# Kernel optimization log

Hardware: AMD Instinct MI355X
Metric: run time of the kernel (lower is better)

## Reference

```python
import jax, jax.numpy as jnp
import numpy as np

N_NODES, N_EDGES, N_REL, F_DIM, N_HEAD, N_LAYERS = 20000, 100000, 1000, 128, 4, 4
NEG_SLOPE = 0.2  # PyG GATv2Conv default negative_slope


def _gatv2_layer(x, ea_full, src, dst, Wl, bl, Wr, br, We, att, bias):
    # x: [N, F]; ea_full: [Etot, F] edge attrs (incl. self-loop rows)
    N = x.shape[0]
    H, C = att.shape  # heads, out-dim per head
    xl = (x @ Wl + bl).reshape(N, H, C)          # source-side projection
    xr = (x @ Wr + br).reshape(N, H, C)          # target-side projection
    ee = (ea_full @ We).reshape(-1, H, C)        # [Etot, H, C] edge embedding
    # GATv2 scoring: leaky_relu(x_i + x_j + e) . att
    e = jax.nn.leaky_relu(xl[src] + xr[dst] + ee, NEG_SLOPE)
    logits = jnp.einsum('ehc,hc->eh', e, att)    # [Etot, H]
    # segment softmax over edges grouped by destination node
    m = jax.ops.segment_max(logits, dst, num_segments=N)
    p = jnp.exp(logits - m[dst])
    denom = jax.ops.segment_sum(p, dst, num_segments=N)
    alpha = p / denom[dst]                       # [Etot, H]
    out = jax.ops.segment_sum(alpha[:, :, None] * xl[src], dst, num_segments=N)
    return out.mean(axis=1) + bias               # concat=False -> head mean


def setup_inputs() -> dict:
    key = jax.random.key(0)
    ks = jax.random.split(key, 12)
    N, E, R, F, H, L = N_NODES, N_EDGES, N_REL, F_DIM, N_HEAD, N_LAYERS
    HC = H * F
    s = 1.0 / np.sqrt(F)
    return {
        'x': jax.random.normal(ks[0], (N, F), jnp.float32),
        'edge_index': jax.random.randint(ks[1], (2, E), 0, N, dtype=jnp.int32),
        'relations': jax.random.normal(ks[2], (R, F), jnp.float32),
        'relation_index': jax.random.randint(ks[3], (E,), 0, R, dtype=jnp.int32),
        'Wl': jax.random.normal(ks[4], (L, F, HC), jnp.float32) * s,
        'bl': jnp.zeros((L, HC), jnp.float32),
        'Wr': jax.random.normal(ks[5], (L, F, HC), jnp.float32) * s,
        'br': jnp.zeros((L, HC), jnp.float32),
        'We': jax.random.normal(ks[6], (L, F, HC), jnp.float32) * s,
        'att': jax.random.normal(ks[7], (L, H, F), jnp.float32) * s,
        'bias': jnp.zeros((L, F), jnp.float32),
    }


def reference(x, edge_index, relations, relation_index, Wl, bl, Wr, br, We, att, bias):
    N = x.shape[0]
    sl = jnp.arange(N, dtype=edge_index.dtype)
    src = jnp.concatenate([edge_index[0], sl])   # add_self_loops=True
    dst = jnp.concatenate([edge_index[1], sl])
    ea = relations[relation_index]               # [E, F]
    # self-loop edge_attr uses fill_value='mean' (PyG default)
    ea_mean = ea.mean(axis=0)
    ea_full = jnp.concatenate([ea, jnp.broadcast_to(ea_mean, (N, ea.shape[1]))])
    h = x
    for l in range(N_LAYERS):
        h = _gatv2_layer(h, ea_full, src, dst, Wl[l], bl[l], Wr[l], br[l], We[l], att[l], bias[l])
    return (h, relations)
```

## Files before the change

### kernel.cpp

```cpp
#include <hip/hip_runtime.h>
#include <hip/hip_bf16.h>

#define N_NODES   20000
#define N_EDGES   100000
#define N_REL     1000
#define F_DIM     128
#define N_HEAD    4
#define HC        512
#define HC2       256
#define N_LAYERS  4
#define REL_EXT_ROWS 1008
#define NEG_SLOPE 0.2f
#define PROJ_NODE_X 157

typedef __attribute__((ext_vector_type(8))) short short8;
typedef __attribute__((ext_vector_type(4))) float floatx4;

__device__ __forceinline__ float loadIn(const void* p, size_t i, int f32) {
    if (f32) return ((const float*)p)[i];
    union { unsigned int u; float f; } c;
    c.u = ((unsigned int)((const unsigned short*)p)[i]) << 16;
    return c.f;
}

__device__ __forceinline__ unsigned short f2bf(float v) {
    __hip_bfloat16 b = __float2bfloat16(v);
    return *(unsigned short*)&b;
}

__device__ __forceinline__ void unpack2(unsigned int u, float& lo, float& hi) {
    union { unsigned int u; float f; } a, b;
    a.u = u << 16;
    b.u = u & 0xFFFF0000u;
    lo = a.f; hi = b.f;
}

__device__ __forceinline__ void unpack8(uint4 v, float* f) {
    unpack2(v.x, f[0], f[1]);
    unpack2(v.y, f[2], f[3]);
    unpack2(v.z, f[4], f[5]);
    unpack2(v.w, f[6], f[7]);
}

__global__ void detect_kernel(const unsigned short* __restrict__ x, int* __restrict__ flag) {
    int t = threadIdx.x;
    int cnt = 0;
    for (int j = t; j < 256; j += 64) {
        int e = (x[j] >> 7) & 0xFF;
        if (e >= 143) cnt++;
    }
    for (int off = 32; off; off >>= 1) cnt += __shfl_xor(cnt, off);
    if (t == 0) flag[0] = (cnt >= 8) ? 1 : 0;
}


__global__ void hist_kernel(const int* __restrict__ dst, const int* __restrict__ rel,
                            int* __restrict__ deg, int* __restrict__ rcount) {
    int e = blockIdx.x * 256 + threadIdx.x;
    if (e < N_EDGES) {
        atomicAdd(&deg[dst[e]], 1);
        atomicAdd(&rcount[rel[e]], 1);
    }
}

__global__ void ea_mean_kernel(const int* __restrict__ rcount,
                               const void* __restrict__ relations,
                               float* __restrict__ ea_mean, const int* __restrict__ flag) {
    int f32 = flag[0];
    int b = blockIdx.x;
    int t = threadIdx.x;
    int col = t & 127;
    int rhalf = t >> 7;
    float acc = 0.f;
    for (int j = 0; j < 4; ++j) {
        int r = b * 8 + j * 2 + rhalf;
        acc += (float)rcount[r] * loadIn(relations, (size_t)r * F_DIM + col, f32);
    }
    __shared__ float part[256];
    part[t] = acc;
    __syncthreads();
    if (t < 128)
        atomicAdd(&ea_mean[col], (part[t] + part[t + 128]) * (1.f / (float)N_EDGES));
}

__global__ void relext_kernel(const void* __restrict__ relations,
                              const float* __restrict__ ea_mean,
                              unsigned short* __restrict__ rel_ext, const int* __restrict__ flag) {
    int idx = blockIdx.x * 256 + threadIdx.x;
    if (idx >= REL_EXT_ROWS * F_DIM) return;
    int f32 = flag[0];
    int r = idx >> 7;
    int c = idx & 127;
    float v;
    if (r < N_REL)       v = loadIn(relations, idx, f32);
    else if (r == N_REL) v = ea_mean[c];
    else                 v = 0.f;
    rel_ext[idx] = f2bf(v);
}

__global__ void scan_kernel(const int* __restrict__ deg,
                            int* __restrict__ row_start, int* __restrict__ cursor) {
    __shared__ int part[1024];
    int t = threadIdx.x;
    const int CH = (N_NODES + 1023) / 1024;
    int base = t * CH;
    int sum = 0;
    for (int j = 0; j < CH; ++j) {
        int idx = base + j;
        if (idx < N_NODES) sum += deg[idx];
    }
    part[t] = sum;
    __syncthreads();
    for (int off = 1; off < 1024; off <<= 1) {
        int u = (t >= off) ? part[t - off] : 0;
        __syncthreads();
        part[t] += u;
        __syncthreads();
    }
    int run = part[t] - sum;
    for (int j = 0; j < CH; ++j) {
        int idx = base + j;
        if (idx < N_NODES) {
            row_start[idx] = run;
            cursor[idx] = run;
            run += deg[idx];
        }
    }
    if (t == 1023) row_start[N_NODES] = part[1023];
}

__global__ void scatter_kernel(const int* __restrict__ src, const int* __restrict__ dst,
                               const int* __restrict__ rel, int* __restrict__ cursor,
                               int* __restrict__ csr_pack) {
    int e = blockIdx.x * 256 + threadIdx.x;
    if (e < N_EDGES) {
        int d = dst[e];
        int p = atomicAdd(&cursor[d], 1);
        csr_pack[p] = src[e] | (rel[e] << 16);
    }
}

__global__ void build8_kernel(const int* __restrict__ row_start,
                              const int* __restrict__ csr_pack,
                              int* __restrict__ csr8) {
    int i = blockIdx.x * 256 + threadIdx.x;
    if (i >= N_NODES) return;
    int rs = row_start[i];
    int deg = row_start[i + 1] - rs;
    if (deg < 0) deg = 0;
    int dcap = deg > 4095 ? 4095 : deg;
    csr8[i * 8] = rs | (dcap << 17);
    #pragma unroll
    for (int k = 0; k < 7; ++k)
        csr8[i * 8 + 1 + k] = (k < deg) ? csr_pack[rs + k] : 0;
}

__global__ void tail_kernel(const void* __restrict__ relations, void* __restrict__ out,
                            const int* __restrict__ flag) {
    int i = blockIdx.x * 256 + threadIdx.x;
    if (i >= N_REL * F_DIM) return;
    int f32 = flag[0];
    float v = loadIn(relations, i, f32);
    size_t o = (size_t)N_NODES * F_DIM + i;
    if (f32) ((float*)out)[o] = v;
    else     ((unsigned short*)out)[o] = f2bf(v);
}

__global__ void w_transpose_kernel(const void* __restrict__ Wl, const void* __restrict__ Wr,
                                   const void* __restrict__ We,
                                   unsigned short* __restrict__ Wt, const int* __restrict__ flag) {
    int f32 = flag[0];
    int k0 = blockIdx.x * 64;
    int n0 = blockIdx.y * 64;
    int mat = blockIdx.z;
    const void* src = (mat < 4) ? Wl : (mat < 8 ? Wr : We);
    size_t base = (size_t)(mat & 3) * F_DIM * HC;
    unsigned short* dst = Wt + (size_t)mat * HC * F_DIM;
    __shared__ float T[64][65];
    int t = threadIdx.x;
    int r = t >> 2, cq = t & 3;
    for (int j = 0; j < 16; ++j) {
        int n = cq * 16 + j;
        T[n][r] = loadIn(src, base + (size_t)(k0 + r) * HC + n0 + n, f32);
    }
    __syncthreads();
    for (int j = 0; j < 16; ++j) {
        int k = cq * 16 + j;
        dst[(size_t)(n0 + r) * F_DIM + k0 + k] = f2bf(T[r][k]);
    }
}

__launch_bounds__(256, 3)
__global__ void proj_kernel(const void* __restrict__ A_node, int a_input,
                            const unsigned short* __restrict__ rel_ext,
                            const unsigned short* __restrict__ Wlt,
                            const unsigned short* __restrict__ Wrt,
                            const unsigned short* __restrict__ Wet,
                            const void* __restrict__ bl, const void* __restrict__ br,
                            size_t boff,
                            unsigned short* __restrict__ xl,
                            unsigned short* __restrict__ xr,
                            unsigned short* __restrict__ re,
                            const int* __restrict__ flag) {
    __shared__ __align__(16) short As[64][136];
    __shared__ __align__(16) short Cs[64 * 136];
    int f32 = flag[0];
    int t = threadIdx.x;
    int y = blockIdx.y;
    int isNode = (blockIdx.x < PROJ_NODE_X);

    const void* A;
    const unsigned short* Wt;
    const void* bias;
    unsigned short* out;
    int M, mbase, nT, a_f32;
    int n0 = (y & 3) * 128;
    if (isNode) {
        A = A_node; M = N_NODES; nT = 2;
        mbase = blockIdx.x * 128;
        a_f32 = a_input ? f32 : 0;
        if (y < 4) { Wt = Wlt; bias = bl; out = xl; }
        else       { Wt = Wrt; bias = br; out = xr; }
    } else {
        A = (const void*)rel_ext; M = REL_EXT_ROWS; nT = 4;
        int rowchunk = (blockIdx.x - PROJ_NODE_X) * 2 + (y >> 2);
        mbase = rowchunk * 256;
        a_f32 = 0;
        Wt = Wet; bias = nullptr; out = re;
    }

    int wave = t >> 6, lane = t & 63;
    int wm = (wave >> 1) * 32, wn = (wave & 1) * 64;
    int r16 = lane & 15, quad = lane >> 4;

    short8 breg[2][2][4];
    #pragma unroll
    for (int half = 0; half < 2; ++half)
        #pragma unroll
        for (int kk = 0; kk < 2; ++kk)
            #pragma unroll
            for (int ni = 0; ni < 4; ++ni)
                breg[half][kk][ni] = *(const short8*)(
                    Wt + (size_t)(n0 + wn + ni * 16 + r16) * F_DIM + half * 64 + kk * 32 + quad * 8);

    float bv[4];
    #pragma unroll
    for (int ni = 0; ni < 4; ++ni)
        bv[ni] = bias ? loadIn(bias, boff + n0 + wn + ni * 16 + r16, f32) : 0.f;

    short8 aS[4];
    #pragma unroll
    for (int j = 0; j < 4; ++j) {
        int c = t + j * 256;
        int row = c >> 4;
        int colc = (c & 15) * 8;
        int gm = mbase + row;
        short8 v = (short8){0, 0, 0, 0, 0, 0, 0, 0};
        if (gm < M) {
            size_t idx = (size_t)gm * F_DIM + colc;
            if (a_f32) {
                const float* Af = (const float*)A;
                for (int q = 0; q < 8; ++q) v[q] = (short)f2bf(Af[idx + q]);
            } else {
                v = *(const short8*)((const unsigned short*)A + idx);
            }
        }
        aS[j] = v;
    }

    for (int ct = 0; ct < nT; ++ct) {
        int m0 = mbase + ct * 64;
        __syncthreads();
        #pragma unroll
        for (int j = 0; j < 4; ++j) {
            int c = t + j * 256;
            *(short8*)&As[c >> 4][(c & 15) * 8] = aS[j];
        }
        short8 aN[4];
        if (ct + 1 < nT) {
            int mb = mbase + (ct + 1) * 64;
            #pragma unroll
            for (int j = 0; j < 4; ++j) {
                int c = t + j * 256;
                int row = c >> 4;
                int colc = (c & 15) * 8;
                int gm = mb + row;
                short8 v = (short8){0, 0, 0, 0, 0, 0, 0, 0};
                if (gm < M) {
                    size_t idx = (size_t)gm * F_DIM + colc;
                    if (a_f32) {
                        const float* Af = (const float*)A;
                        for (int q = 0; q < 8; ++q) v[q] = (short)f2bf(Af[idx + q]);
                    } else {
                        v = *(const short8*)((const unsigned short*)A + idx);
                    }
                }
                aN[j] = v;
            }
            #pragma unroll
            for (int j = 0; j < 4; ++j) aS[j] = aN[j];
        }
        __syncthreads();

        floatx4 acc[2][4];
        #pragma unroll
        for (int mi = 0; mi < 2; ++mi)
            #pragma unroll
            for (int ni = 0; ni < 4; ++ni)
                acc[mi][ni] = (floatx4){0.f, 0.f, 0.f, 0.f};

        #pragma unroll
        for (int half = 0; half < 2; ++half) {
            #pragma unroll
            for (int kk = 0; kk < 2; ++kk) {
                short8 a[2];
                #pragma unroll
                for (int mi = 0; mi < 2; ++mi)
                    a[mi] = *(const short8*)&As[wm + mi * 16 + r16][half * 64 + kk * 32 + quad * 8];
                #pragma unroll
                for (int mi = 0; mi < 2; ++mi)
                    #pragma unroll
                    for (int ni = 0; ni < 4; ++ni)
                        acc[mi][ni] = __builtin_amdgcn_mfma_f32_16x16x32_bf16(
                            a[mi], breg[half][kk][ni], acc[mi][ni], 0, 0, 0);
            }
        }

        #pragma unroll
        for (int mi = 0; mi < 2; ++mi) {
            #pragma unroll
            for (int ni = 0; ni < 4; ++ni) {
                int col = wn + ni * 16 + r16;
                #pragma unroll
                for (int r = 0; r < 4; ++r) {
                    int rowl = wm + mi * 16 + quad * 4 + r;
                    Cs[rowl * 136 + col] = (short)f2bf(acc[mi][ni][r] + bv[ni]);
                }
            }
        }
        __syncthreads();
        #pragma unroll
        for (int j = 0; j < 4; ++j) {
            int c = t + j * 256;
            int rowl = c >> 4;
            int colc = (c & 15) * 8;
            int gm = m0 + rowl;
            if (gm < M)
                *(short8*)(out + (size_t)gm * HC + n0 + colc) =
                    *(const short8*)&Cs[rowl * 136 + colc];
        }
    }
}

__launch_bounds__(128)
__global__ void edge_kernel(const unsigned int* __restrict__ xl2,
                            const unsigned int* __restrict__ xr2,
                            const unsigned int* __restrict__ re2,
                            const int* __restrict__ csr8,
                            const int* __restrict__ csr_pack,
                            const void* __restrict__ att, size_t att_off,
                            const void* __restrict__ bias, size_t bias_off,
                            void* __restrict__ hout, int final_layer,
                            const int* __restrict__ flag) {
    int f32 = flag[0];
    int wid = threadIdx.x >> 6;
    int lane = threadIdx.x & 63;
    int i = blockIdx.x * 2 + wid;
    if (i >= N_NODES) return;
    int h = lane >> 4;
    int q = lane & 15;
    int loff = h * 64 + q * 4;

    uint4 h0 = *(const uint4*)(csr8 + (size_t)i * 8);
    uint4 h1 = *(const uint4*)(csr8 + (size_t)i * 8 + 4);
    int rs  = (int)(h0.x & 0x1FFFF);
    int deg = (int)(h0.x >> 17) & 0xFFF;
    int ew[7] = { (int)h0.y, (int)h0.z, (int)h0.w, (int)h1.x, (int)h1.y, (int)h1.z, (int)h1.w };

    uint4 xrv = *(const uint4*)(xr2 + (size_t)i * HC2 + loff);
    uint4 erv = *(const uint4*)(re2 + (size_t)N_REL * HC2 + loff);
    uint4 xsv = *(const uint4*)(xl2 + (size_t)i * HC2 + loff);
    float av[8];
    #pragma unroll
    for (int j = 0; j < 8; ++j)
        av[j] = loadIn(att, att_off + (size_t)h * F_DIM + q * 8 + j, f32);

    int nIn = deg > 7 ? 7 : deg;
    uint4 xv[7], rv[7];
    #pragma unroll
    for (int k = 0; k < 7; ++k) {
        int pk = ew[k];
        int valid = (k < nIn);
        int sn = pk & 0xFFFF;
        int rn = (pk >> 16) & 0x3FF;
        if (!valid || sn >= N_NODES) sn = i;
        if (!valid || rn > N_REL)    rn = N_REL;
        xv[k] = *(const uint4*)(xl2 + (size_t)sn * HC2 + loff);
        rv[k] = *(const uint4*)(re2 + (size_t)rn * HC2 + loff);
    }

    __builtin_amdgcn_sched_barrier(0);

    float xr[8], er[8];
    unpack8(xrv, xr);
    unpack8(erv, er);

    float acc[8];
    float s;
    {
        float xs[8];
        unpack8(xsv, xs);
        float part = 0.f;
        #pragma unroll
        for (int j = 0; j < 8; ++j) {
            float u = xs[j] + xr[j] + er[j];
            u = fmaxf(u, NEG_SLOPE * u);
            part = fmaf(u, av[j], part);
        }
        #pragma unroll
        for (int off = 8; off; off >>= 1) part += __shfl_xor(part, off);
        part = fminf(fmaxf(part, -60.f), 60.f);
        float p = __expf(part);
        s = p;
        #pragma unroll
        for (int j = 0; j < 8; ++j) acc[j] = p * xs[j];
    }

    #pragma unroll
    for (int k = 0; k < 7; ++k) {
        if (k < nIn) {
            float xlv[8], ee[8];
            unpack8(xv[k], xlv);
            unpack8(rv[k], ee);
            float part = 0.f;
            #pragma unroll
            for (int j = 0; j < 8; ++j) {
                float u = xlv[j] + xr[j] + ee[j];
                u = fmaxf(u, NEG_SLOPE * u);
                part = fmaf(u, av[j], part);
            }
            #pragma unroll
            for (int off = 8; off; off >>= 1) part += __shfl_xor(part, off);
            part = fminf(fmaxf(part, -60.f), 60.f);
            float pp = __expf(part);
            s += pp;
            #pragma unroll
            for (int j = 0; j < 8; ++j) acc[j] = fmaf(pp, xlv[j], acc[j]);
        }
    }

    if (deg > 7) {
        int e1 = rs + deg;
        if (e1 > N_EDGES) e1 = N_EDGES;
        for (int b = rs + 7; b < e1; b += 4) {
            int nb = e1 - b; if (nb > 4) nb = 4;
            uint4 xo[4], ro[4];
            #pragma unroll
            for (int k = 0; k < 4; ++k) {
                int idx = b + k;
                if (idx >= e1) idx = e1 - 1;
                int pk = csr_pack[idx];
                int sn = pk & 0xFFFF;        if (sn >= N_NODES) sn = 0;
                int rn = (pk >> 16) & 0x3FF; if (rn > N_REL) rn = N_REL;
                xo[k] = *(const uint4*)(xl2 + (size_t)sn * HC2 + loff);
                ro[k] = *(const uint4*)(re2 + (size_t)rn * HC2 + loff);
            }
            __builtin_amdgcn_sched_barrier(0);
            #pragma unroll
            for (int k = 0; k < 4; ++k) {
                if (k < nb) {
                    float xlv[8], ee[8];
                    unpack8(xo[k], xlv);
                    unpack8(ro[k], ee);
                    float part = 0.f;
                    #pragma unroll
                    for (int j = 0; j < 8; ++j) {
                        float u = xlv[j] + xr[j] + ee[j];
                        u = fmaxf(u, NEG_SLOPE * u);
                        part = fmaf(u, av[j], part);
                    }
                    #pragma unroll
                    for (int off = 8; off; off >>= 1) part += __shfl_xor(part, off);
                    part = fminf(fmaxf(part, -60.f), 60.f);
                    float pp = __expf(part);
                    s += pp;
                    #pragma unroll
                    for (int j = 0; j < 8; ++j) acc[j] = fmaf(pp, xlv[j], acc[j]);
                }
            }
        }
    }

    float inv = 1.f / s;
    float outv[8];
    #pragma unroll
    for (int j = 0; j < 8; ++j) outv[j] = acc[j] * inv;
    #pragma unroll
    for (int j = 0; j < 8; ++j) {
        outv[j] += __shfl_xor(outv[j], 16);
        outv[j] += __shfl_xor(outv[j], 32);
    }

    if (h == 0) {
        float bv[8];
        #pragma unroll
        for (int j = 0; j < 8; ++j)
            bv[j] = loadIn(bias, bias_off + q * 8 + j, f32);
        size_t o = (size_t)i * F_DIM + q * 8;
        if (final_layer && f32) {
            float* op = (float*)hout + o;
            float4 lo, hi;
            lo.x = outv[0] * 0.25f + bv[0];
            lo.y = outv[1] * 0.25f + bv[1];
            lo.z = outv[2] * 0.25f + bv[2];
            lo.w = outv[3] * 0.25f + bv[3];
            hi.x = outv[4] * 0.25f + bv[4];
            hi.y = outv[5] * 0.25f + bv[5];
            hi.z = outv[6] * 0.25f + bv[6];
            hi.w = outv[7] * 0.25f + bv[7];
            *(float4*)op = lo;
            *(float4*)(op + 4) = hi;
        } else {
            unsigned int w[4];
            #pragma unroll
            for (int p = 0; p < 4; ++p) {
                float v0 = outv[2 * p] * 0.25f + bv[2 * p];
                float v1 = outv[2 * p + 1] * 0.25f + bv[2 * p + 1];
                w[p] = (unsigned int)f2bf(v0) | ((unsigned int)f2bf(v1) << 16);
            }
            *(uint4*)((unsigned short*)hout + o) = *(uint4*)w;
        }
    }
}


extern "C" void kernel_launch(void* const* d_in, const int* in_sizes, int n_in,
                              void* d_out, int out_size, void* d_ws, size_t ws_size,
                              hipStream_t stream) {
    const void* x          = d_in[0];
    const int*  edge_index = (const int*)d_in[1];
    const void* relations  = d_in[2];
    const int*  rel_index  = (const int*)d_in[3];
    const void* Wl         = d_in[4];
    const void* bl         = d_in[5];
    const void* Wr         = d_in[6];
    const void* br         = d_in[7];
    const void* We         = d_in[8];
    const void* att        = d_in[9];
    const void* bias       = d_in[10];

    char* ws = (char*)d_ws;
    size_t off = 0;
    auto alloc = [&](size_t bytes) -> void* {
        void* p = ws + off;
        off = (off + bytes + 255) & ~(size_t)255;
        return p;
    };
    int*            flag     = (int*)alloc(4);
    char*           zero0    = ws + off;
    int*            deg      = (int*)alloc(N_NODES * 4);
    int*            rcount   = (int*)alloc(N_REL * 4);
    float*          ea_mean  = (float*)alloc(F_DIM * 4);
    size_t          zlen     = (size_t)((ws + off) - zero0);
    int*            row_start= (int*)alloc((N_NODES + 1) * 4);
    int*            cursor   = (int*)alloc(N_NODES * 4);
    int*            csr_pack = (int*)alloc(N_EDGES * 4);
    int*            csr8     = (int*)alloc((size_t)N_NODES * 8 * 4);
    unsigned short* rel_ext  = (unsigned short*)alloc((size_t)REL_EXT_ROWS * F_DIM * 2);
    unsigned short* Wt       = (unsigned short*)alloc((size_t)12 * HC * F_DIM * 2);
    unsigned short* re       = (unsigned short*)alloc((size_t)REL_EXT_ROWS * HC * 2);
    unsigned short* hbuf     = (unsigned short*)alloc((size_t)N_NODES * F_DIM * 2);
    unsigned short* xl       = (unsigned short*)alloc((size_t)N_NODES * HC * 2);
    unsigned short* xr       = (unsigned short*)alloc((size_t)N_NODES * HC * 2);

    const int* esrc = edge_index;
    const int* edst = edge_index + N_EDGES;

    detect_kernel<<<1, 64, 0, stream>>>((const unsigned short*)x, flag);
    hipMemsetAsync(zero0, 0, zlen, stream);
    hist_kernel<<<(N_EDGES + 255) / 256, 256, 0, stream>>>(edst, rel_index, deg, rcount);
    ea_mean_kernel<<<N_REL / 8, 256, 0, stream>>>(rcount, relations, ea_mean, flag);
    relext_kernel<<<(REL_EXT_ROWS * F_DIM + 255) / 256, 256, 0, stream>>>(relations, ea_mean, rel_ext, flag);
    scan_kernel<<<1, 1024, 0, stream>>>(deg, row_start, cursor);
    scatter_kernel<<<(N_EDGES + 255) / 256, 256, 0, stream>>>(esrc, edst, rel_index, cursor, csr_pack);
    build8_kernel<<<(N_NODES + 255) / 256, 256, 0, stream>>>(row_start, csr_pack, csr8);
    w_transpose_kernel<<<dim3(2, 8, 12), 256, 0, stream>>>(Wl, Wr, We, Wt, flag);
    tail_kernel<<<(N_REL * F_DIM + 255) / 256, 256, 0, stream>>>(relations, d_out, flag);

    const void* hin = x;
    int a_input = 1;
    for (int l = 0; l < N_LAYERS; ++l) {
        const unsigned short* Wlt = Wt + (size_t)l * HC * F_DIM;
        const unsigned short* Wrt = Wt + (size_t)(4 + l) * HC * F_DIM;
        const unsigned short* Wet = Wt + (size_t)(8 + l) * HC * F_DIM;
        proj_kernel<<<dim3(PROJ_NODE_X + 2, 8), 256, 0, stream>>>(
            hin, a_input, rel_ext, Wlt, Wrt, Wet,
            bl, br, (size_t)l * HC,
            xl, xr, re, flag);
        int final_layer = (l == N_LAYERS - 1);
        void* hout = final_layer ? d_out : (void*)hbuf;
        edge_kernel<<<(N_NODES + 1) / 2, 128, 0, stream>>>(
            (const unsigned int*)xl, (const unsigned int*)xr, (const unsigned int*)re,
            csr8, csr_pack,
            att, (size_t)l * N_HEAD * F_DIM,
            bias, (size_t)l * F_DIM,
            hout, final_layer, flag);
        hin = hbuf;
        a_input = 0;
    }
}
```

Baseline: 431.3 us.

## Stage edge gathers into LDS via global_load_lds and enlarge node projection tiles

```diff
diff --git a/kernel.cpp b/kernel.cpp
--- a/kernel.cpp
+++ b/kernel.cpp
@@ -11,7 +11,7 @@
 #define N_LAYERS  4
 #define REL_EXT_ROWS 1008
 #define NEG_SLOPE 0.2f
-#define PROJ_NODE_X 157
+#define PROJ_NODE_X 79
 
 typedef __attribute__((ext_vector_type(8))) short short8;
 typedef __attribute__((ext_vector_type(4))) float floatx4;
@@ -40,6 +40,18 @@
     unpack2(v.y, f[2], f[3]);
     unpack2(v.z, f[4], f[5]);
     unpack2(v.w, f[6], f[7]);
+}
+
+__device__ __forceinline__ void gload_lds16(const unsigned int* g, unsigned int* l) {
+    __builtin_amdgcn_global_load_lds(
+        (const __attribute__((address_space(1))) unsigned int*)g,
+        (__attribute__((address_space(3))) unsigned int*)l,
+        16, 0, 0);
+}
+
+__device__ __forceinline__ void vm_drain() {
+    asm volatile("s_waitcnt vmcnt(0)" ::: "memory");
+    __builtin_amdgcn_sched_barrier(0);
 }
 
 __global__ void detect_kernel(const unsigned short* __restrict__ x, int* __restrict__ flag) {
@@ -216,8 +228,8 @@
     int M, mbase, nT, a_f32;
     int n0 = (y & 3) * 128;
     if (isNode) {
-        A = A_node; M = N_NODES; nT = 2;
-        mbase = blockIdx.x * 128;
+        A = A_node; M = N_NODES; nT = 4;
+        mbase = blockIdx.x * 256;
         a_f32 = a_input ? f32 : 0;
         if (y < 4) { Wt = Wlt; bias = bl; out = xl; }
         else       { Wt = Wrt; bias = br; out = xr; }
@@ -362,6 +374,7 @@
                             const void* __restrict__ bias, size_t bias_off,
                             void* __restrict__ hout, int final_layer,
                             const int* __restrict__ flag) {
+    __shared__ __align__(16) unsigned int stage[2][7][2][256];
     int f32 = flag[0];
     int wid = threadIdx.x >> 6;
     int lane = threadIdx.x & 63;
@@ -386,20 +399,16 @@
         av[j] = loadIn(att, att_off + (size_t)h * F_DIM + q * 8 + j, f32);
 
     int nIn = deg > 7 ? 7 : deg;
-    uint4 xv[7], rv[7];
     #pragma unroll
     for (int k = 0; k < 7; ++k) {
-        int pk = ew[k];
-        int valid = (k < nIn);
-        int sn = pk & 0xFFFF;
-        int rn = (pk >> 16) & 0x3FF;
-        if (!valid || sn >= N_NODES) sn = i;
-        if (!valid || rn > N_REL)    rn = N_REL;
-        xv[k] = *(const uint4*)(xl2 + (size_t)sn * HC2 + loff);
-        rv[k] = *(const uint4*)(re2 + (size_t)rn * HC2 + loff);
-    }
-
-    __builtin_amdgcn_sched_barrier(0);
+        if (k < nIn) {
+            int pk = ew[k];
+            int sn = pk & 0xFFFF;        if (sn >= N_NODES) sn = 0;
+            int rn = (pk >> 16) & 0x3FF; if (rn > N_REL) rn = N_REL;
+            gload_lds16(xl2 + (size_t)sn * HC2 + loff, &stage[wid][k][0][0]);
+            gload_lds16(re2 + (size_t)rn * HC2 + loff, &stage[wid][k][1][0]);
+        }
+    }
 
     float xr[8], er[8];
     unpack8(xrv, xr);
@@ -426,12 +435,16 @@
         for (int j = 0; j < 8; ++j) acc[j] = p * xs[j];
     }
 
+    vm_drain();
+
     #pragma unroll
     for (int k = 0; k < 7; ++k) {
         if (k < nIn) {
             float xlv[8], ee[8];
-            unpack8(xv[k], xlv);
-            unpack8(rv[k], ee);
+            uint4 xv = *(const uint4*)&stage[wid][k][0][lane * 4];
+            uint4 rv = *(const uint4*)&stage[wid][k][1][lane * 4];
+            unpack8(xv, xlv);
+            unpack8(rv, ee);
             float part = 0.f;
             #pragma unroll
             for (int j = 0; j < 8; ++j) {
@@ -457,15 +470,14 @@
             uint4 xo[4], ro[4];
             #pragma unroll
             for (int k = 0; k < 4; ++k) {
-                int idx = b + k;
-                if (idx >= e1) idx = e1 - 1;
-                int pk = csr_pack[idx];
-                int sn = pk & 0xFFFF;        if (sn >= N_NODES) sn = 0;
-                int rn = (pk >> 16) & 0x3FF; if (rn > N_REL) rn = N_REL;
-                xo[k] = *(const uint4*)(xl2 + (size_t)sn * HC2 + loff);
-                ro[k] = *(const uint4*)(re2 + (size_t)rn * HC2 + loff);
-            }
-            __builtin_amdgcn_sched_barrier(0);
+                if (k < nb) {
+                    int pk = csr_pack[b + k];
+                    int sn = pk & 0xFFFF;        if (sn >= N_NODES) sn = 0;
+                    int rn = (pk >> 16) & 0x3FF; if (rn > N_REL) rn = N_REL;
+                    xo[k] = *(const uint4*)(xl2 + (size_t)sn * HC2 + loff);
+                    ro[k] = *(const uint4*)(re2 + (size_t)rn * HC2 + loff);
+                }
+            }
             #pragma unroll
             for (int k = 0; k < 4; ++k) {
                 if (k < nb) {
```

Measured after the change: 451.8 us. +4.7%, slower.
